# Optimization experiments

Hardware: AMD Instinct MI355X
Metric: run time of the kernel (lower is better)

Reference implementation:

```python
import jax, jax.numpy as jnp
import numpy as np

B, N, D, A = 4, 4096, 512, 64

def setup_inputs() -> dict:
    key = jax.random.key(0)
    ks = jax.random.split(key, 7)
    s = 1.0 / np.sqrt(D)
    return {
        "inputs": jax.random.normal(ks[0], (B, N, D), dtype=jnp.float32),
        "Wq": jax.random.normal(ks[1], (D, A), dtype=jnp.float32) * s,
        "bq": jnp.zeros((A,), dtype=jnp.float32),
        "Wk": jax.random.normal(ks[2], (D, A), dtype=jnp.float32) * s,
        "bk": jnp.zeros((A,), dtype=jnp.float32),
        "Wv": jax.random.normal(ks[3], (D, A), dtype=jnp.float32) * s,
        "bv": jnp.zeros((A,), dtype=jnp.float32),
    }

def reference(inputs, Wq, bq, Wk, bk, Wv, bv):
    # Dense projections: [B,N,D] @ [D,A] + [A] -> [B,N,A]
    Q = jnp.einsum('bnd,da->bna', inputs, Wq) + bq
    K = jnp.einsum('bnd,da->bna', inputs, Wk) + bk
    V = jnp.einsum('bnd,da->bna', inputs, Wv) + bv
    scale = 1.0 / jnp.sqrt(jnp.float32(A))
    scores = jnp.einsum('bqa,bka->bqk', Q, K) * scale  # [B,N,N]
    weights = jax.nn.softmax(scores, axis=-1)
    return jnp.einsum('bqk,bka->bqa', weights, V)  # [B,N,A]
```

## Files before the change

### kernel.cpp

```cpp
#include <hip/hip_runtime.h>
#include <hip/hip_bf16.h>

namespace {

constexpr int Bn = 4, Nn = 4096, An = 64;

typedef __attribute__((ext_vector_type(8))) short bf16x8;
typedef __attribute__((ext_vector_type(4))) float f32x4;

constexpr float QSCALE = 0.125f * 1.4426950408889634f;

__device__ __forceinline__ short f2bf(float f) {
    __hip_bfloat16 h = __float2bfloat16(f);
    return *reinterpret_cast<short*>(&h);
}
__device__ __forceinline__ float bf2f(short s) {
    unsigned u = ((unsigned)(unsigned short)s) << 16;
    return *reinterpret_cast<float*>(&u);
}
__device__ __forceinline__ unsigned cvt_pk_bf16(float a, float b) {
    unsigned r;
    asm("v_cvt_pk_bf16_f32 %0, %1, %2" : "=v"(r) : "v"(a), "v"(b));
    return r;
}
__device__ __forceinline__ float hw_exp2(float x) {
    return __builtin_amdgcn_exp2f(x);
}

__global__ __launch_bounds__(256) void wpack(
    const float* __restrict__ Wq, const float* __restrict__ bq,
    const float* __restrict__ Wk, const float* __restrict__ bk,
    const float* __restrict__ Wv, const float* __restrict__ bv,
    short* __restrict__ Wt, float* __restrict__ bc)
{
    const int tid = blockIdx.x * 256 + threadIdx.x;
    const int c = tid >> 6, k0 = (tid & 63) << 3;
    const int m = c >> 6, a = c & 63;
    const float* W = (m == 0) ? Wq : (m == 1) ? Wk : Wv;
    const float s = (m == 0) ? QSCALE : 1.0f;
    bf16x8 o;
    #pragma unroll
    for (int j = 0; j < 8; ++j) o[j] = f2bf(W[(size_t)(k0 + j) * 64 + a] * s);
    *reinterpret_cast<bf16x8*>(Wt + (size_t)c * 512 + k0) = o;
    if (tid < 192) bc[tid] = (m == 0) ? bq[a] * QSCALE : (m == 1) ? bk[a] : bv[a];
}

__global__ __launch_bounds__(512, 2) void qkv_mm(
    const float* __restrict__ x, const short* __restrict__ Wt,
    const float* __restrict__ bc,
    __hip_bfloat16* __restrict__ Qb, __hip_bfloat16* __restrict__ Kb,
    __hip_bfloat16* __restrict__ Vt)
{
    __shared__ __align__(16) short wls[96 * 512];

    const int tid  = threadIdx.x;
    const int w    = tid >> 6, lane = tid & 63;
    const int lo   = lane & 15, g = lane >> 4;
    const int rowgrp = blockIdx.x >> 1;
    const int colgrp = blockIdx.x & 1;
    const int r0   = rowgrp * 128;
    const int c0   = colgrp * 96;

    {
        const uint4* wsrc = reinterpret_cast<const uint4*>(Wt + (size_t)c0 * 512);
        uint4* wdst = reinterpret_cast<uint4*>(wls);
        #pragma unroll
        for (int i = 0; i < 12; ++i) {
            int idx = i * 512 + tid;
            int c = idx >> 6, slot = idx & 63;
            wdst[c * 64 + (slot ^ (c & 7))] = wsrc[idx];
        }
    }
    __syncthreads();

    const int myrow = r0 + w * 16 + lo;
    const float* xr = x + (size_t)myrow * 512 + 8 * g;

    f32x4 acc[6];
    #pragma unroll
    for (int i = 0; i < 6; ++i) acc[i] = f32x4{0.f, 0.f, 0.f, 0.f};

    #pragma unroll 4
    for (int kt = 0; kt < 512; kt += 32) {
        float4 a0 = *reinterpret_cast<const float4*>(xr + kt);
        float4 a1 = *reinterpret_cast<const float4*>(xr + kt + 4);
        float xf[8] = {a0.x, a0.y, a0.z, a0.w, a1.x, a1.y, a1.z, a1.w};
        uint4 hv;
        hv.x = cvt_pk_bf16(xf[0], xf[1]); hv.y = cvt_pk_bf16(xf[2], xf[3]);
        hv.z = cvt_pk_bf16(xf[4], xf[5]); hv.w = cvt_pk_bf16(xf[6], xf[7]);
        bf16x8 ah = *reinterpret_cast<bf16x8*>(&hv);
        float rs[8];
        #pragma unroll
        for (int j = 0; j < 8; ++j) rs[j] = xf[j] - bf2f(ah[j]);
        uint4 lv;
        lv.x = cvt_pk_bf16(rs[0], rs[1]); lv.y = cvt_pk_bf16(rs[2], rs[3]);
        lv.z = cvt_pk_bf16(rs[4], rs[5]); lv.w = cvt_pk_bf16(rs[6], rs[7]);
        bf16x8 al = *reinterpret_cast<bf16x8*>(&lv);

        const int slot = (kt >> 3) + g;
        #pragma unroll
        for (int ct = 0; ct < 6; ++ct) {
            int c = ct * 16 + lo;
            const bf16x8 wf = *reinterpret_cast<const bf16x8*>(
                wls + c * 512 + ((slot ^ (c & 7)) << 3));
            acc[ct] = __builtin_amdgcn_mfma_f32_16x16x32_bf16(ah, wf, acc[ct], 0, 0, 0);
            acc[ct] = __builtin_amdgcn_mfma_f32_16x16x32_bf16(al, wf, acc[ct], 0, 0, 0);
        }
    }

    const int bb = r0 >> 12;
    #pragma unroll
    for (int ct = 0; ct < 6; ++ct) {
        const int gc = c0 + ct * 16 + lo;
        if (colgrp == 1 && ct >= 2) break;
        const float bias = bc[gc];
        __hip_bfloat16* dst = (gc < 64) ? Qb : Kb;
        const int oc = (gc < 64) ? gc : gc - 64;
        #pragma unroll
        for (int r = 0; r < 4; ++r) {
            short hv2 = f2bf(acc[ct][r] + bias);
            dst[(size_t)(r0 + w * 16 + 4 * g + r) * 64 + oc] =
                *reinterpret_cast<__hip_bfloat16*>(&hv2);
        }
    }
    if (colgrp == 1) {
        __syncthreads();
        short* vt = wls + w * 1024;
        #pragma unroll
        for (int ct = 2; ct < 6; ++ct) {
            const int vc = (ct - 2) * 16 + lo;
            const float bias = bc[128 + vc];
            #pragma unroll
            for (int r = 0; r < 4; ++r)
                vt[(4 * g + r) * 64 + vc] = f2bf(acc[ct][r] + bias);
        }
        asm volatile("s_waitcnt lgkmcnt(0)" ::: "memory");
        __builtin_amdgcn_sched_barrier(0);
        unsigned u[8];
        #pragma unroll
        for (int n = 0; n < 8; ++n) {
            unsigned v0 = (unsigned short)vt[(2 * n) * 64 + lane];
            unsigned v1 = (unsigned short)vt[(2 * n + 1) * 64 + lane];
            u[n] = v0 | (v1 << 16);
        }
        const int n0w = (r0 & 4095) + w * 16;
        uint4* dstv = reinterpret_cast<uint4*>(&Vt[((size_t)(bb * 64 + lane)) * 4096 + n0w]);
        dstv[0] = uint4{u[0], u[1], u[2], u[3]};
        dstv[1] = uint4{u[4], u[5], u[6], u[7]};
    }
}

template<int WAVES, int KS, bool DIRECT>
__global__ __launch_bounds__(WAVES * 64, 2) void attn(
    const __hip_bfloat16* __restrict__ Qb,
    const __hip_bfloat16* __restrict__ Kb,
    const __hip_bfloat16* __restrict__ Vt,
    short* __restrict__ Pacc, float* __restrict__ Lbuf, float* __restrict__ outD)
{
    constexpr int T    = WAVES * 64;
    constexpr int QPB  = WAVES * 32;
    constexpr int SBPB = Nn / QPB;
    constexpr int NC   = 512 / T;

    __shared__ __align__(16) short Klds[2][64 * 64];
    __shared__ __align__(16) short Vlds[2][64 * 64];
    __shared__ __align__(16) short Plds[WAVES][2][16 * 64];

    const int tid  = threadIdx.x;
    const int w    = tid >> 6, lane = tid & 63;
    const int lo   = lane & 15, g = lane >> 4;
    const int qsb  = blockIdx.x / KS;
    const int ks   = blockIdx.x % KS;
    const int b    = qsb / SBPB;
    const int nqb  = (qsb % SBPB) * QPB;
    const int k0b  = ks * (Nn / KS);
    const int nsteps = (Nn / KS) / 64;

    bf16x8 qf[2][2];
    #pragma unroll
    for (int qt = 0; qt < 2; ++qt)
        #pragma unroll
        for (int dh = 0; dh < 2; ++dh)
            qf[qt][dh] = *reinterpret_cast<const bf16x8*>(
                &Qb[(size_t)(b * Nn + nqb + w * 32 + qt * 16 + lo) * 64 + dh * 32 + 8 * g]);

    f32x4 acc[2][4];
    #pragma unroll
    for (int q = 0; q < 2; ++q)
        #pragma unroll
        for (int a = 0; a < 4; ++a) acc[q][a] = f32x4{0.f, 0.f, 0.f, 0.f};
    float lsum[2] = {0.f, 0.f};

    uint4 kr[NC], vr[NC];
    auto stg_issue = [&](int s) {
        int k0 = k0b + s * 64;
        #pragma unroll
        for (int i = 0; i < NC; ++i) {
            int c = i * T + tid, key = c >> 3, sl = c & 7;
            kr[i] = *reinterpret_cast<const uint4*>(&Kb[(size_t)(b * Nn + k0 + key) * 64 + sl * 8]);
            vr[i] = *reinterpret_cast<const uint4*>(&Vt[(size_t)(b * 64 + key) * Nn + k0 + sl * 8]);
        }
    };
    auto stg_write = [&](int buf) {
        #pragma unroll
        for (int i = 0; i < NC; ++i) {
            int c = i * T + tid, key = c >> 3, ss = (c & 7) ^ (key & 7);
            *reinterpret_cast<uint4*>(&Klds[buf][key * 64 + ss * 8]) = kr[i];
            *reinterpret_cast<uint4*>(&Vlds[buf][key * 64 + ss * 8]) = vr[i];
        }
    };

    auto step = [&](int buf) {
        bf16x8 ka[4][2], va[4][2];
        #pragma unroll
        for (int t = 0; t < 4; ++t)
            #pragma unroll
            for (int dh = 0; dh < 2; ++dh) {
                int row = lo + 16 * t, ss = (g + 4 * dh) ^ (row & 7);
                ka[t][dh] = *reinterpret_cast<const bf16x8*>(&Klds[buf][row * 64 + ss * 8]);
            }
        #pragma unroll
        for (int at = 0; at < 4; ++at)
            #pragma unroll
            for (int c = 0; c < 2; ++c) {
                int row = at * 16 + lo, ss = (4 * c + g) ^ (row & 7);
                va[at][c] = *reinterpret_cast<const bf16x8*>(&Vlds[buf][row * 64 + ss * 8]);
            }

        f32x4 cc[2][4];
        __builtin_amdgcn_s_setprio(1);
        #pragma unroll
        for (int qt = 0; qt < 2; ++qt)
            #pragma unroll
            for (int t = 0; t < 4; ++t) {
                f32x4 c = f32x4{0.f, 0.f, 0.f, 0.f};
                c = __builtin_amdgcn_mfma_f32_16x16x32_bf16(ka[t][0], qf[qt][0], c, 0, 0, 0);
                c = __builtin_amdgcn_mfma_f32_16x16x32_bf16(ka[t][1], qf[qt][1], c, 0, 0, 0);
                cc[qt][t] = c;
            }
        __builtin_amdgcn_s_setprio(0);

        #pragma unroll
        for (int qt = 0; qt < 2; ++qt) {
            char* pbase = reinterpret_cast<char*>(&Plds[w][qt][0]) + lo * 128;
            #pragma unroll
            for (int t = 0; t < 4; ++t) {
                float p0 = hw_exp2(cc[qt][t][0]), p1 = hw_exp2(cc[qt][t][1]);
                float p2 = hw_exp2(cc[qt][t][2]), p3 = hw_exp2(cc[qt][t][3]);
                lsum[qt] += (p0 + p1) + (p2 + p3);
                uint2 pw = {cvt_pk_bf16(p0, p1), cvt_pk_bf16(p2, p3)};
                int byte = (32 * t + 8 * g) ^ ((lo & 7) << 4);
                *reinterpret_cast<uint2*>(pbase + byte) = pw;
            }
        }
        asm volatile("s_waitcnt lgkmcnt(0)" ::: "memory");

        #pragma unroll
        for (int qt = 0; qt < 2; ++qt) {
            char* pbase = reinterpret_cast<char*>(&Plds[w][qt][0]) + lo * 128;
            bf16x8 pb[2];
            #pragma unroll
            for (int c = 0; c < 2; ++c) {
                int byte = (64 * c + 16 * g) ^ ((lo & 7) << 4);
                pb[c] = *reinterpret_cast<const bf16x8*>(pbase + byte);
            }
            __builtin_amdgcn_s_setprio(1);
            #pragma unroll
            for (int at = 0; at < 4; ++at) {
                acc[qt][at] = __builtin_amdgcn_mfma_f32_16x16x32_bf16(va[at][0], pb[0], acc[qt][at], 0, 0, 0);
                acc[qt][at] = __builtin_amdgcn_mfma_f32_16x16x32_bf16(va[at][1], pb[1], acc[qt][at], 0, 0, 0);
            }
            __builtin_amdgcn_s_setprio(0);
        }
    };

    stg_issue(0);
    stg_write(0);
    __syncthreads();
    for (int s = 0; s < nsteps; ++s) {
        if (s + 1 < nsteps) stg_issue(s + 1);
        step(s & 1);
        if (s + 1 < nsteps) {
            stg_write((s + 1) & 1);
            __syncthreads();
        }
    }

    #pragma unroll
    for (int qt = 0; qt < 2; ++qt) {
        float l = lsum[qt];
        l += __shfl_xor(l, 16);
        l += __shfl_xor(l, 32);
        const int n = nqb + w * 32 + qt * 16 + lo;
        const size_t ng = (size_t)b * Nn + n;
        if (!DIRECT) {
            if (g == 0) Lbuf[(size_t)ks * (Bn * Nn) + ng] = l;
            short* prow = Pacc + ((size_t)ks * (Bn * Nn) + ng) * 64;
            #pragma unroll
            for (int at = 0; at < 4; ++at) {
                uint2 pw = {cvt_pk_bf16(acc[qt][at][0], acc[qt][at][1]),
                            cvt_pk_bf16(acc[qt][at][2], acc[qt][at][3])};
                *reinterpret_cast<uint2*>(prow + at * 16 + 4 * g) = pw;
            }
        } else {
            float inv = 1.0f / l;
            #pragma unroll
            for (int at = 0; at < 4; ++at)
                #pragma unroll
                for (int r = 0; r < 4; ++r)
                    outD[ng * 64 + at * 16 + 4 * g + r] = acc[qt][at][r] * inv;
        }
    }
}

__global__ __launch_bounds__(256) void reduce_out(
    const short* __restrict__ Pacc, const float* __restrict__ Lbuf,
    float* __restrict__ out, int KS)
{
    const int idx = blockIdx.x * 256 + threadIdx.x;
    const int ng  = idx >> 4;
    const int a4  = (idx & 15) * 4;
    float s0 = 0.f, s1 = 0.f, s2 = 0.f, s3 = 0.f, l = 0.f;
    for (int k = 0; k < KS; ++k) {
        uint2 pv = *reinterpret_cast<const uint2*>(
            Pacc + ((size_t)k * (Bn * Nn) + ng) * 64 + a4);
        s0 += bf2f((short)(pv.x & 0xffff));
        s1 += bf2f((short)(pv.x >> 16));
        s2 += bf2f((short)(pv.y & 0xffff));
        s3 += bf2f((short)(pv.y >> 16));
        l  += Lbuf[(size_t)k * (Bn * Nn) + ng];
    }
    const float inv = 1.0f / l;
    float4 o;
    o.x = s0 * inv; o.y = s1 * inv; o.z = s2 * inv; o.w = s3 * inv;
    *reinterpret_cast<float4*>(&out[(size_t)ng * 64 + a4]) = o;
}

}

extern "C" void kernel_launch(void* const* d_in, const int* in_sizes, int n_in,
                              void* d_out, int out_size, void* d_ws, size_t ws_size,
                              hipStream_t stream) {
    const float* x  = (const float*)d_in[0];
    const float* Wq = (const float*)d_in[1];
    const float* bq = (const float*)d_in[2];
    const float* Wk = (const float*)d_in[3];
    const float* bk = (const float*)d_in[4];
    const float* Wv = (const float*)d_in[5];
    const float* bv = (const float*)d_in[6];
    float* out = (float*)d_out;

    char* ws = (char*)d_ws;
    const size_t mat_bytes = (size_t)Bn * Nn * An * sizeof(__hip_bfloat16);
    __hip_bfloat16* Qb = (__hip_bfloat16*)(ws);
    __hip_bfloat16* Kb = (__hip_bfloat16*)(ws + mat_bytes);
    __hip_bfloat16* Vt = (__hip_bfloat16*)(ws + 2 * mat_bytes);
    short* Pacc = (short*)(ws + 3 * mat_bytes);
    const size_t pacc_bytes = (size_t)Bn * An * Nn * sizeof(short);
    const size_t lbuf_per   = (size_t)Bn * Nn * sizeof(float);

    short* Wt = (short*)d_out;
    float* bc = (float*)((char*)d_out + 192 * 512 * 2);

    wpack<<<dim3(48), dim3(256), 0, stream>>>(Wq, bq, Wk, bk, Wv, bv, Wt, bc);
    qkv_mm<<<dim3(256), dim3(512), 0, stream>>>(x, Wt, bc, Qb, Kb, Vt);

    const size_t base = 3 * mat_bytes;
    const int rgrid = (Bn * Nn * An) / (4 * 256);
    if (ws_size >= base + 4 * (pacc_bytes + lbuf_per)) {
        float* Lbuf = (float*)(ws + base + 4 * pacc_bytes);
        attn<8, 4, false><<<dim3((Bn * Nn / 256) * 4), dim3(512), 0, stream>>>(Qb, Kb, Vt, Pacc, Lbuf, out);
        reduce_out<<<dim3(rgrid), dim3(256), 0, stream>>>(Pacc, Lbuf, out, 4);
    } else if (ws_size >= base + 2 * (pacc_bytes + lbuf_per)) {
        float* Lbuf = (float*)(ws + base + 2 * pacc_bytes);
        attn<4, 2, false><<<dim3((Bn * Nn / 128) * 2), dim3(256), 0, stream>>>(Qb, Kb, Vt, Pacc, Lbuf, out);
        reduce_out<<<dim3(rgrid), dim3(256), 0, stream>>>(Pacc, Lbuf, out, 2);
    } else {
        attn<4, 1, true><<<dim3(Bn * Nn / 128), dim3(256), 0, stream>>>(Qb, Kb, Vt, nullptr, nullptr, out);
    }
}
```

Before: 52.96 us.

## Split QKV projection block over columns in-block and pipeline weight staging in halves

```diff
diff --git a/kernel.cpp b/kernel.cpp
--- a/kernel.cpp
+++ b/kernel.cpp
@@ -51,60 +51,81 @@
     __hip_bfloat16* __restrict__ Qb, __hip_bfloat16* __restrict__ Kb,
     __hip_bfloat16* __restrict__ Vt)
 {
-    __shared__ __align__(16) short wls[96 * 512];
+    __shared__ __align__(16) short wls[192 * 256];
 
     const int tid  = threadIdx.x;
     const int w    = tid >> 6, lane = tid & 63;
     const int lo   = lane & 15, g = lane >> 4;
-    const int rowgrp = blockIdx.x >> 1;
-    const int colgrp = blockIdx.x & 1;
-    const int r0   = rowgrp * 128;
-    const int c0   = colgrp * 96;
-
-    {
-        const uint4* wsrc = reinterpret_cast<const uint4*>(Wt + (size_t)c0 * 512);
-        uint4* wdst = reinterpret_cast<uint4*>(wls);
+    const int rg   = w >> 1, cg = w & 1;
+    const int r0   = blockIdx.x * 64;
+    const int c0   = cg * 96;
+
+    const int myrow = r0 + rg * 16 + lo;
+    const float* xr = x + (size_t)myrow * 512 + 8 * g;
+
+    uint4 wreg[12];
+    auto wissue = [&](int ph) {
         #pragma unroll
         for (int i = 0; i < 12; ++i) {
             int idx = i * 512 + tid;
-            int c = idx >> 6, slot = idx & 63;
-            wdst[c * 64 + (slot ^ (c & 7))] = wsrc[idx];
-        }
-    }
+            int c = idx >> 5, slot = idx & 31;
+            wreg[i] = *reinterpret_cast<const uint4*>(
+                Wt + (size_t)c * 512 + ph * 256 + slot * 8);
+        }
+    };
+    auto wwrite = [&]() {
+        uint4* wdst = reinterpret_cast<uint4*>(wls);
+        #pragma unroll
+        for (int i = 0; i < 12; ++i) {
+            int idx = i * 512 + tid;
+            int c = idx >> 5, slot = idx & 31;
+            wdst[c * 32 + (slot ^ (c & 7))] = wreg[i];
+        }
+    };
+
+    f32x4 acc[6];
+    #pragma unroll
+    for (int i = 0; i < 6; ++i) acc[i] = f32x4{0.f, 0.f, 0.f, 0.f};
+
+    wissue(0);
+    wwrite();
     __syncthreads();
-
-    const int myrow = r0 + w * 16 + lo;
-    const float* xr = x + (size_t)myrow * 512 + 8 * g;
-
-    f32x4 acc[6];
-    #pragma unroll
-    for (int i = 0; i < 6; ++i) acc[i] = f32x4{0.f, 0.f, 0.f, 0.f};
-
-    #pragma unroll 4
-    for (int kt = 0; kt < 512; kt += 32) {
-        float4 a0 = *reinterpret_cast<const float4*>(xr + kt);
-        float4 a1 = *reinterpret_cast<const float4*>(xr + kt + 4);
-        float xf[8] = {a0.x, a0.y, a0.z, a0.w, a1.x, a1.y, a1.z, a1.w};
-        uint4 hv;
-        hv.x = cvt_pk_bf16(xf[0], xf[1]); hv.y = cvt_pk_bf16(xf[2], xf[3]);
-        hv.z = cvt_pk_bf16(xf[4], xf[5]); hv.w = cvt_pk_bf16(xf[6], xf[7]);
-        bf16x8 ah = *reinterpret_cast<bf16x8*>(&hv);
-        float rs[8];
-        #pragma unroll
-        for (int j = 0; j < 8; ++j) rs[j] = xf[j] - bf2f(ah[j]);
-        uint4 lv;
-        lv.x = cvt_pk_bf16(rs[0], rs[1]); lv.y = cvt_pk_bf16(rs[2], rs[3]);
-        lv.z = cvt_pk_bf16(rs[4], rs[5]); lv.w = cvt_pk_bf16(rs[6], rs[7]);
-        bf16x8 al = *reinterpret_cast<bf16x8*>(&lv);
-
-        const int slot = (kt >> 3) + g;
-        #pragma unroll
-        for (int ct = 0; ct < 6; ++ct) {
-            int c = ct * 16 + lo;
-            const bf16x8 wf = *reinterpret_cast<const bf16x8*>(
-                wls + c * 512 + ((slot ^ (c & 7)) << 3));
-            acc[ct] = __builtin_amdgcn_mfma_f32_16x16x32_bf16(ah, wf, acc[ct], 0, 0, 0);
-            acc[ct] = __builtin_amdgcn_mfma_f32_16x16x32_bf16(al, wf, acc[ct], 0, 0, 0);
+    wissue(1);
+
+    #pragma unroll
+    for (int ph = 0; ph < 2; ++ph) {
+        #pragma unroll 2
+        for (int kk = 0; kk < 256; kk += 32) {
+            const int kt = ph * 256 + kk;
+            float4 a0 = *reinterpret_cast<const float4*>(xr + kt);
+            float4 a1 = *reinterpret_cast<const float4*>(xr + kt + 4);
+            float xf[8] = {a0.x, a0.y, a0.z, a0.w, a1.x, a1.y, a1.z, a1.w};
+            uint4 hv;
+            hv.x = cvt_pk_bf16(xf[0], xf[1]); hv.y = cvt_pk_bf16(xf[2], xf[3]);
+            hv.z = cvt_pk_bf16(xf[4], xf[5]); hv.w = cvt_pk_bf16(xf[6], xf[7]);
+            bf16x8 ah = *reinterpret_cast<bf16x8*>(&hv);
+            float rs[8];
+            #pragma unroll
+            for (int j = 0; j < 8; ++j) rs[j] = xf[j] - bf2f(ah[j]);
+            uint4 lv;
+            lv.x = cvt_pk_bf16(rs[0], rs[1]); lv.y = cvt_pk_bf16(rs[2], rs[3]);
+            lv.z = cvt_pk_bf16(rs[4], rs[5]); lv.w = cvt_pk_bf16(rs[6], rs[7]);
+            bf16x8 al = *reinterpret_cast<bf16x8*>(&lv);
+
+            const int slot = (kk >> 3) + g;
+            #pragma unroll
+            for (int ct = 0; ct < 6; ++ct) {
+                int c = c0 + ct * 16 + lo;
+                const bf16x8 wf = *reinterpret_cast<const bf16x8*>(
+                    wls + c * 256 + ((slot ^ (c & 7)) << 3));
+                acc[ct] = __builtin_amdgcn_mfma_f32_16x16x32_bf16(ah, wf, acc[ct], 0, 0, 0);
+                acc[ct] = __builtin_amdgcn_mfma_f32_16x16x32_bf16(al, wf, acc[ct], 0, 0, 0);
+            }
+        }
+        if (ph == 0) {
+            __syncthreads();
+            wwrite();
+            __syncthreads();
         }
     }
 
@@ -112,19 +133,19 @@
     #pragma unroll
     for (int ct = 0; ct < 6; ++ct) {
         const int gc = c0 + ct * 16 + lo;
-        if (colgrp == 1 && ct >= 2) break;
+        if (cg == 1 && ct >= 2) break;
         const float bias = bc[gc];
         __hip_bfloat16* dst = (gc < 64) ? Qb : Kb;
         const int oc = (gc < 64) ? gc : gc - 64;
         #pragma unroll
         for (int r = 0; r < 4; ++r) {
             short hv2 = f2bf(acc[ct][r] + bias);
-            dst[(size_t)(r0 + w * 16 + 4 * g + r) * 64 + oc] =
+            dst[(size_t)(r0 + rg * 16 + 4 * g + r) * 64 + oc] =
                 *reinterpret_cast<__hip_bfloat16*>(&hv2);
         }
     }
-    if (colgrp == 1) {
-        __syncthreads();
+    __syncthreads();
+    if (cg == 1) {
         short* vt = wls + w * 1024;
         #pragma unroll
         for (int ct = 2; ct < 6; ++ct) {
@@ -143,7 +164,7 @@
             unsigned v1 = (unsigned short)vt[(2 * n + 1) * 64 + lane];
             u[n] = v0 | (v1 << 16);
         }
-        const int n0w = (r0 & 4095) + w * 16;
+        const int n0w = (r0 & 4095) + rg * 16;
         uint4* dstv = reinterpret_cast<uint4*>(&Vt[((size_t)(bb * 64 + lane)) * 4096 + n0w]);
         dstv[0] = uint4{u[0], u[1], u[2], u[3]};
         dstv[1] = uint4{u[4], u[5], u[6], u[7]};
```

Result: slower. 65.86 us (+24.4%).
